# Optimization experiments

Measured on AMD Instinct MI355X. Metric: run time of the kernel, lower is better.

The kernel has to match this reference:

```python
import jax, jax.numpy as jnp
import numpy as np
from jax import lax

B, N, S, K = 8, 8192, 1024, 32
R2 = 0.2 ** 2
EPS = 1e-5


def _gather(p, idx):
    # p: [B, N, C]; idx: [B, ...] int -> p[b, idx[b]]
    bidx = jnp.arange(p.shape[0]).reshape((p.shape[0],) + (1,) * (idx.ndim - 1))
    return p[bidx, idx]


def _fps(xyz):
    # farthest point sampling; deterministic start at index 0 (torch version uses randint)
    def step(carry, _):
        dist, far = carry
        c = _gather(xyz, far[:, None])            # [B,1,3]
        d = jnp.sum((xyz - c) ** 2, -1)           # [B,N]
        dist = jnp.minimum(dist, d)
        return (dist, jnp.argmax(dist, -1).astype(jnp.int32)), far
    init = (jnp.full(xyz.shape[:2], 1e10, xyz.dtype), jnp.zeros((xyz.shape[0],), jnp.int32))
    _, idx = lax.scan(step, init, None, length=S)
    return idx.T                                   # [B,S]


def _ball_query(xyz, new_xyz):
    # squared dists [B,S,N]
    sq = (jnp.sum(new_xyz ** 2, -1)[:, :, None] + jnp.sum(xyz ** 2, -1)[:, None, :]
          - 2.0 * jnp.einsum('bsc,bnc->bsn', new_xyz, xyz))
    gi = jnp.where(sq > R2, N, jnp.arange(N, dtype=jnp.int32))
    # K smallest indices within radius == K largest of (N - gi); equivalent to sort()[:, :, :K]
    vals, _ = lax.top_k(N - gi, K)
    gi = N - vals                                  # [B,S,K]
    first = gi[:, :, :1]
    return jnp.where(gi == N, first, gi)


def _forward(xyz, points, params):
    xyz = xyz.transpose(0, 2, 1)                   # [B,N,3]
    points = points.transpose(0, 2, 1)             # [B,N,C]
    fps_idx = _fps(xyz)                            # [B,S]
    new_xyz = _gather(xyz, fps_idx)                # [B,S,3]
    gi = _ball_query(xyz, new_xyz)                 # [B,S,K]
    g_xyz = _gather(xyz, gi) - new_xyz[:, :, None, :]            # [B,S,K,3]
    g_pts = jnp.concatenate([_gather(points, gi), g_xyz], -1)    # [B,S,K,C+3]
    x = g_pts.transpose(0, 3, 2, 1)                # [B,C+3,K,S]
    for w, b, g, be in params:
        x = jnp.einsum('oc,bcks->boks', w, x) + b[None, :, None, None]
        m = jnp.mean(x, axis=(0, 2, 3), keepdims=True)
        v = jnp.mean((x - m) ** 2, axis=(0, 2, 3), keepdims=True)  # biased var (BN train mode)
        x = jax.nn.relu(g[None, :, None, None] * (x - m) / jnp.sqrt(v + EPS) + be[None, :, None, None])
    return new_xyz.transpose(0, 2, 1), jnp.max(x, axis=2)          # [B,3,S], [B,128,S]


def setup_inputs() -> dict:
    key = jax.random.key(0)
    ks = jax.random.split(key, 8)
    chans = [(67, 64), (64, 64), (64, 128)]
    inp = {
        'xyz': jax.random.normal(ks[0], (B, 3, N), jnp.float32),
        'points': jax.random.normal(ks[1], (B, 64, N), jnp.float32),
    }
    for i, (ci, co) in enumerate(chans):
        kw = jax.random.fold_in(ks[2], i)
        inp[f'w{i}'] = jax.random.normal(kw, (co, ci), jnp.float32) * 0.1
        inp[f'b{i}'] = jnp.zeros((co,), jnp.float32)
        inp[f'g{i}'] = jnp.ones((co,), jnp.float32)
        inp[f'be{i}'] = jnp.zeros((co,), jnp.float32)
    return inp


def reference(xyz, points, w0, b0, g0, be0, w1, b1, g1, be1, w2, b2, g2, be2):
    params = [(w0, b0, g0, be0), (w1, b1, g1, be1), (w2, b2, g2, be2)]
    return _forward(xyz, points, params)
```

## Files before the change

kernel.cpp:

```cpp
#include <hip/hip_runtime.h>

typedef unsigned short ushort_t;
typedef unsigned int uint_t;
typedef unsigned long long u64_t;
typedef unsigned short us8 __attribute__((ext_vector_type(8)));

constexpr int B_ = 8, N_ = 8192, S_ = 1024, K_ = 32;
constexpr int M_ = B_ * S_ * K_;
constexpr float R2_ = 0.04f;
constexpr float EPS_ = 1e-5f;

__device__ __forceinline__ float bf2f(ushort_t u) {
    union { uint_t i; float f; } v; v.i = ((uint_t)u) << 16; return v.f;
}
__device__ __forceinline__ ushort_t f2bf(float f) {
    union { float f; uint_t i; } v; v.f = f;
    uint_t i = v.i;
    uint_t r = (i + 0x7FFFu + ((i >> 16) & 1u)) >> 16;
    return (ushort_t)r;
}

template<int C> __device__ __forceinline__ float dmaxf(float v) {
    int o = __builtin_amdgcn_mov_dpp(__float_as_int(v), C, 0xf, 0xf, true);
    return fmaxf(v, __int_as_float(o));
}

__global__ __launch_bounds__(1024, 4)
void fps_kernel(const float* __restrict__ xyz, int* __restrict__ fps_idx) {
    constexpr int T = 1024, P = N_ / T;
    const int b = blockIdx.x, t = threadIdx.x;
    const int lane = t & 63, w = t >> 6;
    const float* X = xyz + (size_t)b * 3 * N_;

    __shared__ float4 sxyz[N_];
    __shared__ float rv[16];
    __shared__ int sfar;

#pragma unroll
    for (int i = 0; i < P; ++i) {
        int n = t + i * T;
        sxyz[n] = make_float4(X[n], X[N_ + n], X[2 * N_ + n], 0.0f);
    }
    if (t == 0) fps_idx[b * S_] = 0;
    __syncthreads();

    float px[P], py[P], pz[P], dist[P];
#pragma unroll
    for (int i = 0; i < P; ++i) {
        float4 v = sxyz[t * P + i];
        px[i] = v.x; py[i] = v.y; pz[i] = v.z;
        dist[i] = 1e10f;
    }
    float4 cc = sxyz[0];
    float cx = cc.x, cy = cc.y, cz = cc.z;

    for (int s = 0; s < S_; ++s) {
#pragma unroll
        for (int i = 0; i < P; ++i) {
            float dx = __fsub_rn(px[i], cx);
            float dy = __fsub_rn(py[i], cy);
            float dz = __fsub_rn(pz[i], cz);
            float d = __fadd_rn(__fadd_rn(__fmul_rn(dx, dx), __fmul_rn(dy, dy)), __fmul_rn(dz, dz));
            dist[i] = fminf(dist[i], d);
        }
        float a0 = fmaxf(dist[0], dist[4]);
        float a1 = fmaxf(dist[1], dist[5]);
        float a2 = fmaxf(dist[2], dist[6]);
        float a3 = fmaxf(dist[3], dist[7]);
        float lmax = fmaxf(fmaxf(a0, a1), fmaxf(a2, a3));
        float m = lmax;
        m = dmaxf<0x111>(m);
        m = dmaxf<0x112>(m);
        m = dmaxf<0x114>(m);
        m = dmaxf<0x118>(m);
        m = dmaxf<0x142>(m);
        m = dmaxf<0x143>(m);
        if (lane == 63) rv[w] = m;
        __syncthreads();

        float kv0 = rv[lane & 15];
        float kv = kv0;
        kv = dmaxf<0x121>(kv);
        kv = dmaxf<0x122>(kv);
        kv = dmaxf<0x124>(kv);
        kv = dmaxf<0x128>(kv);
        float gmax = kv;
        u64_t wm = __ballot(kv0 == gmax);
        int first_w = __builtin_ctzll(wm);

        if (w == first_w) {
            u64_t lm = __ballot(lmax == gmax);
            int L = __builtin_ctzll(lm);
            if (lane == L) {
                int fi = 0;
#pragma unroll
                for (int i = P - 1; i >= 0; --i)
                    if (dist[i] == gmax) fi = i;
                int nf = t * P + fi;
                sfar = nf;
                if (s + 1 < S_) fps_idx[b * S_ + s + 1] = nf;
            }
        }
        __syncthreads();
        int nf = sfar;
        float4 c = sxyz[nf];
        cx = c.x; cy = c.y; cz = c.z;
    }
}

__global__ __launch_bounds__(256)
void gather_nxyz(const float* __restrict__ xyz, const int* __restrict__ fps_idx,
                 float* __restrict__ nxyz, float* __restrict__ out0) {
    int i = blockIdx.x * 256 + threadIdx.x;
    if (i >= B_ * S_) return;
    int b = i / S_, s = i % S_;
    int idx = fps_idx[i];
    const float* X = xyz + (size_t)b * 3 * N_;
    float x = X[idx], y = X[N_ + idx], z = X[2 * N_ + idx];
    nxyz[(size_t)i * 3 + 0] = x;
    nxyz[(size_t)i * 3 + 1] = y;
    nxyz[(size_t)i * 3 + 2] = z;
    out0[((size_t)b * 3 + 0) * S_ + s] = x;
    out0[((size_t)b * 3 + 1) * S_ + s] = y;
    out0[((size_t)b * 3 + 2) * S_ + s] = z;
}

__global__ __launch_bounds__(256)
void ballq_kernel(const float* __restrict__ xyz, const float* __restrict__ nxyz,
                  int* __restrict__ gi) {
    int wid = (blockIdx.x * 256 + threadIdx.x) >> 6;
    int lane = threadIdx.x & 63;
    if (wid >= B_ * S_) return;
    int b = wid / S_;
    const float* X = xyz + (size_t)b * 3 * N_;
    float nx = nxyz[(size_t)wid * 3 + 0];
    float ny = nxyz[(size_t)wid * 3 + 1];
    float nz = nxyz[(size_t)wid * 3 + 2];
    float snew = __fadd_rn(__fadd_rn(__fmul_rn(nx, nx), __fmul_rn(ny, ny)), __fmul_rn(nz, nz));
    int cnt = 0; int firstn = 0;
    int* out = gi + (size_t)wid * K_;
    for (int c0 = 0; c0 < N_; c0 += 64) {
        int n = c0 + lane;
        float xx = X[n], xy = X[N_ + n], xz = X[2 * N_ + n];
        float sxn = __fadd_rn(__fadd_rn(__fmul_rn(xx, xx), __fmul_rn(xy, xy)), __fmul_rn(xz, xz));
        float dot = __fadd_rn(__fadd_rn(__fmul_rn(nx, xx), __fmul_rn(ny, xy)), __fmul_rn(nz, xz));
        float sq = __fsub_rn(__fadd_rn(snew, sxn), __fmul_rn(2.0f, dot));
        bool inr = !(sq > R2_);
        unsigned long long mask = __ballot(inr);
        if (cnt == 0 && mask) firstn = c0 + __builtin_ctzll(mask);
        int rank = __popcll(mask & ((1ull << lane) - 1ull));
        if (inr && cnt + rank < K_) out[cnt + rank] = n;
        cnt += (int)__popcll(mask);
        if (cnt >= K_) break;
    }
    if (cnt < K_ && lane >= cnt && lane < K_) out[lane] = firstn;
}

__global__ __launch_bounds__(256)
void transpose_pts(const float* __restrict__ pts, ushort_t* __restrict__ ptT) {
    __shared__ ushort_t tile[64][66];
    int b = blockIdx.y; int n0 = blockIdx.x * 64;
    int tc = threadIdx.x & 63;
    int tr = threadIdx.x >> 6;
    const float* src = pts + (size_t)b * 64 * N_;
#pragma unroll
    for (int i = 0; i < 16; ++i) {
        int c = i * 4 + tr;
        tile[c][tc] = f2bf(src[(size_t)c * N_ + n0 + tc]);
    }
    __syncthreads();
#pragma unroll
    for (int i = 0; i < 16; ++i) {
        int nr = i * 4 + tr;
        ptT[((size_t)b * N_ + n0 + nr) * 64 + tc] = tile[tc][nr];
    }
}

__global__ void wt_kernel(const float* __restrict__ w0, const float* __restrict__ w1,
                          const float* __restrict__ w2, float* __restrict__ wt) {
    int l = blockIdx.x;
    const float* w = l == 0 ? w0 : (l == 1 ? w1 : w2);
    int CI = (l == 0) ? 67 : 64;
    int CO = (l == 2) ? 128 : 64;
    float* dst = wt + (l == 0 ? 0 : (l == 1 ? 67 * 64 : 67 * 64 + 64 * 64));
    for (int i = threadIdx.x; i < CI * CO; i += 256) {
        int c = i / CO, o = i % CO;
        dst[c * CO + o] = w[o * CI + c];
    }
}

template<bool FUSED>
__global__ __launch_bounds__(256)
void layer_kernel(const ushort_t* __restrict__ xin,
                  const ushort_t* __restrict__ ptT,
                  const float* __restrict__ xyz,
                  const float* __restrict__ nxyz,
                  const int* __restrict__ gi,
                  const float* __restrict__ WT,
                  const float* __restrict__ bias,
                  const float* __restrict__ abuf,
                  ushort_t* __restrict__ y,
                  int COtot) {
    int m = blockIdx.x * 256 + threadIdx.x;
    int os = blockIdx.y * 64;
    float acc[64];
#pragma unroll
    for (int o = 0; o < 64; ++o) acc[o] = bias[os + o];

    int idx = 0, b = 0;
    const ushort_t* row;
    if constexpr (FUSED) {
        idx = gi[m];
        b = m >> 15;
        row = ptT + ((size_t)b * N_ + idx) * 64;
    } else {
        row = xin + (size_t)m * 64;
    }
#pragma unroll
    for (int c8 = 0; c8 < 8; ++c8) {
        us8 v = *reinterpret_cast<const us8*>(row + c8 * 8);
#pragma unroll
        for (int j = 0; j < 8; ++j) {
            int c = c8 * 8 + j;
            float h = bf2f(v[j]);
            if constexpr (!FUSED) h = fmaxf(fmaf(abuf[c], h, abuf[128 + c]), 0.0f);
            const float* wr = WT + (size_t)c * COtot + os;
#pragma unroll
            for (int o = 0; o < 64; ++o) acc[o] = fmaf(h, wr[o], acc[o]);
        }
    }
    if constexpr (FUSED) {
        int s = (m >> 5) & (S_ - 1);
        const float* X = xyz + (size_t)b * 3 * N_;
        const float* nx = nxyz + ((size_t)(b * S_ + s)) * 3;
#pragma unroll
        for (int j = 0; j < 3; ++j) {
            float h = X[(size_t)j * N_ + idx] - nx[j];
            const float* wr = WT + (size_t)(64 + j) * COtot + os;
#pragma unroll
            for (int o = 0; o < 64; ++o) acc[o] = fmaf(h, wr[o], acc[o]);
        }
    }
    ushort_t* yr = y + (size_t)m * COtot + os;
#pragma unroll
    for (int v8 = 0; v8 < 8; ++v8) {
        us8 w;
#pragma unroll
        for (int j = 0; j < 8; ++j) w[j] = f2bf(acc[v8 * 8 + j]);
        *reinterpret_cast<us8*>(yr + v8 * 8) = w;
    }
}

template<int CO>
__global__ __launch_bounds__(256)
void stats_kernel(const ushort_t* __restrict__ y, float* __restrict__ sums) {
    __shared__ float ls[256];
    int t = threadIdx.x;
    ls[t] = 0.0f;
    __syncthreads();
    int lane = t & 63;
    int wid = blockIdx.x * 4 + (t >> 6);
    int nw = gridDim.x * 4;
    if constexpr (CO == 64) {
        float s = 0, q = 0;
        for (int m = wid; m < M_; m += nw) {
            float v = bf2f(y[(size_t)m * 64 + lane]);
            s += v; q = fmaf(v, v, q);
        }
        atomicAdd(&ls[lane], s); atomicAdd(&ls[128 + lane], q);
    } else {
        float s0 = 0, q0 = 0, s1 = 0, q1 = 0;
        for (int m = wid; m < M_; m += nw) {
            uint_t v = *reinterpret_cast<const uint_t*>(y + (size_t)m * 128 + lane * 2);
            float a = bf2f((ushort_t)(v & 0xffff));
            float c = bf2f((ushort_t)(v >> 16));
            s0 += a; q0 = fmaf(a, a, q0);
            s1 += c; q1 = fmaf(c, c, q1);
        }
        int c0 = lane * 2;
        atomicAdd(&ls[c0], s0); atomicAdd(&ls[c0 + 1], s1);
        atomicAdd(&ls[128 + c0], q0); atomicAdd(&ls[128 + c0 + 1], q1);
    }
    __syncthreads();
    atomicAdd(&sums[t], ls[t]);
}

__global__ void finalize_kernel(const float* __restrict__ sums, const float* __restrict__ g,
                                const float* __restrict__ be, float* __restrict__ ab, int CO) {
    int c = threadIdx.x;
    if (c < CO) {
        float mean = sums[c] * (1.0f / (float)M_);
        float var = sums[128 + c] * (1.0f / (float)M_) - mean * mean;
        float a = g[c] / sqrtf(var + EPS_);
        ab[c] = a;
        ab[128 + c] = be[c] - mean * a;
    }
}

__global__ __launch_bounds__(256)
void final_max(const ushort_t* __restrict__ x3, const float* __restrict__ ab,
               float* __restrict__ out1) {
    int t = threadIdx.x;
    int gw = blockIdx.x * 4 + (t >> 6);
    if (gw >= B_ * S_) return;
    int lane = t & 63;
    int b = gw / S_, s = gw % S_;
    int c0 = lane * 2;
    float a0 = ab[c0], k0 = ab[128 + c0];
    float a1 = ab[c0 + 1], k1 = ab[128 + c0 + 1];
    const ushort_t* base = x3 + (size_t)gw * K_ * 128;
    float m0 = -1e30f, m1 = -1e30f;
#pragma unroll 8
    for (int k = 0; k < K_; ++k) {
        uint_t v = *reinterpret_cast<const uint_t*>(base + k * 128 + c0);
        float f0 = fmaf(bf2f((ushort_t)(v & 0xffff)), a0, k0);
        float f1 = fmaf(bf2f((ushort_t)(v >> 16)), a1, k1);
        m0 = fmaxf(m0, f0); m1 = fmaxf(m1, f1);
    }
    out1[((size_t)b * 128 + c0) * S_ + s] = fmaxf(m0, 0.0f);
    out1[((size_t)b * 128 + c0 + 1) * S_ + s] = fmaxf(m1, 0.0f);
}

extern "C" void kernel_launch(void* const* d_in, const int* in_sizes, int n_in,
                              void* d_out, int out_size, void* d_ws, size_t ws_size,
                              hipStream_t stream) {
    const float* xyz = (const float*)d_in[0];
    const float* pts = (const float*)d_in[1];
    const float* w0 = (const float*)d_in[2];
    const float* b0 = (const float*)d_in[3];
    const float* g0 = (const float*)d_in[4];
    const float* be0 = (const float*)d_in[5];
    const float* w1 = (const float*)d_in[6];
    const float* b1 = (const float*)d_in[7];
    const float* g1 = (const float*)d_in[8];
    const float* be1 = (const float*)d_in[9];
    const float* w2 = (const float*)d_in[10];
    const float* b2 = (const float*)d_in[11];
    const float* g2 = (const float*)d_in[12];
    const float* be2 = (const float*)d_in[13];

    float* out0 = (float*)d_out;
    float* out1 = out0 + (size_t)B_ * 3 * S_;

    char* ws = (char*)d_ws;
    int*      fps   = (int*)(ws + 0);
    float*    nxyz  = (float*)(ws + 32768);
    int*      gi    = (int*)(ws + 131072);
    float*    stats = (float*)(ws + 1179648);
    float*    ab    = (float*)(ws + 1182720);
    float*    wt    = (float*)(ws + 1185792);
    ushort_t* ptT   = (ushort_t*)(ws + 2097152);
    ushort_t* xA    = (ushort_t*)(ws + 10485760);
    ushort_t* xB    = (ushort_t*)(ws + 77594624);

    hipMemsetAsync(stats, 0, 3 * 256 * sizeof(float), stream);
    wt_kernel<<<3, 256, 0, stream>>>(w0, w1, w2, wt);
    transpose_pts<<<dim3(N_ / 64, B_), 256, 0, stream>>>(pts, ptT);
    fps_kernel<<<B_, 1024, 0, stream>>>(xyz, fps);
    gather_nxyz<<<(B_ * S_ + 255) / 256, 256, 0, stream>>>(xyz, fps, nxyz, out0);
    ballq_kernel<<<(B_ * S_) / 4, 256, 0, stream>>>(xyz, nxyz, gi);

    layer_kernel<true><<<dim3(M_ / 256, 1), 256, 0, stream>>>(
        xA, ptT, xyz, nxyz, gi, wt, b0, ab, xA, 64);
    stats_kernel<64><<<256, 256, 0, stream>>>(xA, stats + 0);
    finalize_kernel<<<1, 128, 0, stream>>>(stats + 0, g0, be0, ab + 0, 64);

    layer_kernel<false><<<dim3(M_ / 256, 1), 256, 0, stream>>>(
        xA, ptT, xyz, nxyz, gi, wt + 67 * 64, b1, ab + 0, xB, 64);
    stats_kernel<64><<<256, 256, 0, stream>>>(xB, stats + 256);
    finalize_kernel<<<1, 128, 0, stream>>>(stats + 256, g1, be1, ab + 256, 64);

    layer_kernel<false><<<dim3(M_ / 256, 2), 256, 0, stream>>>(
        xB, ptT, xyz, nxyz, gi, wt + 67 * 64 + 64 * 64, b2, ab + 256, xA, 128);
    stats_kernel<128><<<256, 256, 0, stream>>>(xA, stats + 512);
    finalize_kernel<<<1, 128, 0, stream>>>(stats + 512, g2, be2, ab + 512, 128);

    final_max<<<(B_ * S_) / 4, 256, 0, stream>>>(xA, ab + 512, out1);
}
```

Before: 1.402 ms.

## Remove second barrier per FPS step via packed key reduction and double-buffered slots

Result: slower. 1.517 ms (+8.2%).

```diff
diff --git a/kernel.cpp b/kernel.cpp
--- a/kernel.cpp
+++ b/kernel.cpp
@@ -23,6 +23,12 @@
 template<int C> __device__ __forceinline__ float dmaxf(float v) {
     int o = __builtin_amdgcn_mov_dpp(__float_as_int(v), C, 0xf, 0xf, true);
     return fmaxf(v, __int_as_float(o));
+}
+template<int C> __device__ __forceinline__ u64_t dmaxk(u64_t k) {
+    int lo = __builtin_amdgcn_mov_dpp((int)(uint_t)k, C, 0xf, 0xf, true);
+    int hi = __builtin_amdgcn_mov_dpp((int)(uint_t)(k >> 32), C, 0xf, 0xf, true);
+    u64_t o = ((u64_t)(uint_t)hi << 32) | (uint_t)lo;
+    return o > k ? o : k;
 }
 
 __global__ __launch_bounds__(1024, 4)
@@ -33,28 +39,29 @@
     const float* X = xyz + (size_t)b * 3 * N_;
 
     __shared__ float4 sxyz[N_];
-    __shared__ float rv[16];
-    __shared__ int sfar;
+    __shared__ u64_t rk[2][16];
 
 #pragma unroll
     for (int i = 0; i < P; ++i) {
         int n = t + i * T;
         sxyz[n] = make_float4(X[n], X[N_ + n], X[2 * N_ + n], 0.0f);
     }
-    if (t == 0) fps_idx[b * S_] = 0;
     __syncthreads();
 
     float px[P], py[P], pz[P], dist[P];
 #pragma unroll
     for (int i = 0; i < P; ++i) {
-        float4 v = sxyz[t * P + i];
-        px[i] = v.x; py[i] = v.y; pz[i] = v.z;
-        dist[i] = 1e10f;
+        int j = (i + t) & (P - 1);
+        float4 v = sxyz[t * P + j];
+        px[j] = v.x; py[j] = v.y; pz[j] = v.z;
+        dist[j] = 1e10f;
     }
     float4 cc = sxyz[0];
     float cx = cc.x, cy = cc.y, cz = cc.z;
+    int far = 0;
 
     for (int s = 0; s < S_; ++s) {
+        if (t == 0) fps_idx[b * S_ + s] = far;
 #pragma unroll
         for (int i = 0; i < P; ++i) {
             float dx = __fsub_rn(px[i], cx);
@@ -75,35 +82,26 @@
         m = dmaxf<0x118>(m);
         m = dmaxf<0x142>(m);
         m = dmaxf<0x143>(m);
-        if (lane == 63) rv[w] = m;
+        float wmax = __int_as_float(__builtin_amdgcn_readlane(__float_as_int(m), 63));
+        u64_t bal = __ballot(lmax == wmax);
+        int L = __builtin_ctzll(bal);
+        int p = s & 1;
+        if (lane == L) {
+            int fi = 0;
+#pragma unroll
+            for (int i = P - 1; i >= 0; --i)
+                if (dist[i] == wmax) fi = i;
+            uint_t ci = (uint_t)(N_ - 1 - (t * P + fi));
+            rk[p][w] = ((u64_t)(uint_t)__float_as_int(wmax) << 32) | ci;
+        }
         __syncthreads();
-
-        float kv0 = rv[lane & 15];
-        float kv = kv0;
-        kv = dmaxf<0x121>(kv);
-        kv = dmaxf<0x122>(kv);
-        kv = dmaxf<0x124>(kv);
-        kv = dmaxf<0x128>(kv);
-        float gmax = kv;
-        u64_t wm = __ballot(kv0 == gmax);
-        int first_w = __builtin_ctzll(wm);
-
-        if (w == first_w) {
-            u64_t lm = __ballot(lmax == gmax);
-            int L = __builtin_ctzll(lm);
-            if (lane == L) {
-                int fi = 0;
-#pragma unroll
-                for (int i = P - 1; i >= 0; --i)
-                    if (dist[i] == gmax) fi = i;
-                int nf = t * P + fi;
-                sfar = nf;
-                if (s + 1 < S_) fps_idx[b * S_ + s + 1] = nf;
-            }
-        }
-        __syncthreads();
-        int nf = sfar;
-        float4 c = sxyz[nf];
+        u64_t k = rk[p][lane & 15];
+        k = dmaxk<0x121>(k);
+        k = dmaxk<0x122>(k);
+        k = dmaxk<0x124>(k);
+        k = dmaxk<0x128>(k);
+        far = N_ - 1 - (int)(uint_t)k;
+        float4 c = sxyz[far];
         cx = c.x; cy = c.y; cz = c.z;
     }
 }
```
